# Performance work log

Measured on AMD Instinct MI355X. Metric: run time of the kernel, lower is better.

## Reference

```python
import jax, jax.numpy as jnp
import numpy as np

D2 = 200  # 2*D with D=100, hidden size of H and U

def setup_inputs() -> dict:
    key = jax.random.key(0)
    k1, k2, k3, k4 = jax.random.split(key, 4)
    B, T, J = 64, 2048, 128
    H = jax.random.normal(k1, (B, T, D2), dtype=jnp.float32)
    U = jax.random.normal(k2, (B, J, D2), dtype=jnp.float32)
    # alpha = nn.Linear(6D, 1): weight [600], bias scalar
    bound = 1.0 / np.sqrt(6 * 100)
    w = jax.random.uniform(k3, (3 * D2,), minval=-bound, maxval=bound, dtype=jnp.float32)
    b = jax.random.uniform(k4, (), minval=-bound, maxval=bound, dtype=jnp.float32)
    return {"H": H, "U": U, "w": w, "b": b}

def reference(H, U, w, b):
    # Trilinear similarity S[b,t,j] = alpha([H_t; U_j; H_t*U_j]) decomposed:
    # identical math to concat+linear, without materializing [B,T*J,6D].
    w_h, w_u, w_m = w[:D2], w[D2:2 * D2], w[2 * D2:]
    S = (jnp.einsum('btd,d->bt', H, w_h)[:, :, None]
         + jnp.einsum('bjd,d->bj', U, w_u)[:, None, :]
         + jnp.einsum('btd,d,bjd->btj', H, w_m, U)
         + b)  # [B,T,J]
    C2Q_att = jax.nn.softmax(S, axis=-1)            # [B,T,J]
    U_tilde = jnp.einsum('btj,bjd->btd', C2Q_att, U)  # [B,T,2D]
    Q2C_att = jax.nn.softmax(jnp.max(S, axis=-1), axis=-1)  # [B,T]
    H_tilde = jnp.einsum('bt,btd->bd', Q2C_att, H)[:, None, :]  # [B,1,2D]
    T = H.shape[1]
    H_tilde_rep = jnp.broadcast_to(H_tilde, H.shape)  # repeat(1,T,1)
    G = jnp.concatenate([H, U_tilde, H * U_tilde, H * H_tilde_rep], axis=-1)  # [B,T,8D]
    return G, Q2C_att[:, None, :]
```

## Files before the change

kernel.cpp:

```cpp
#include <hip/hip_runtime.h>
#include <math.h>

typedef __attribute__((ext_vector_type(8))) short bf16x8;
typedef __attribute__((ext_vector_type(4))) float f32x4;

#define Bb 64
#define Tt 2048
#define Jj 128
#define Dd 200
#define GD 800
#define TILE 32
#define NT 16
#define ROWS_BLK (TILE*NT)
#define NTH 1024

#define OFF_USH 0u
#define OFF_UJT 57344u
#define OFF_HMS 110592u
#define OFF_PSH 139264u
#define OFF_SUS 147456u
#define OFF_SHS 147968u
#define OFF_SMX 148224u
#define OFF_SSM 149248u
#define SMEM_BYTES 150272u

__device__ __forceinline__ unsigned short f2bf(float f) {
    union { float f; unsigned u; } v; v.f = f;
    unsigned r = v.u + 0x7FFFu + ((v.u >> 16) & 1u);
    return (unsigned short)(r >> 16);
}

__device__ __forceinline__ bf16x8 pack8(f32x4 a, f32x4 b) {
    bf16x8 o;
    o[0] = (short)f2bf(a[0]); o[1] = (short)f2bf(a[1]);
    o[2] = (short)f2bf(a[2]); o[3] = (short)f2bf(a[3]);
    o[4] = (short)f2bf(b[0]); o[5] = (short)f2bf(b[1]);
    o[6] = (short)f2bf(b[2]); o[7] = (short)f2bf(b[3]);
    return o;
}

__device__ __forceinline__ void stage_h(char* smem, const float* __restrict__ Hrows,
                                        int tid, int buf,
                                        f32x4 wmA, f32x4 wmB, f32x4 whA, f32x4 whB)
{
    const int row = tid >> 5, c = tid & 31;
    float shp = 0.f;
    bf16x8 val = {0,0,0,0,0,0,0,0};
    if (c < 25) {
        const float* p = Hrows + row * Dd + c * 8;
        f32x4 h0 = *(const f32x4*)p, h1 = *(const f32x4*)(p + 4);
        shp = h0[0]*whA[0] + h0[1]*whA[1] + h0[2]*whA[2] + h0[3]*whA[3]
            + h1[0]*whB[0] + h1[1]*whB[1] + h1[2]*whB[2] + h1[3]*whB[3];
        val = pack8(h0 * wmA, h1 * wmB);
    }
    if (c < 28) {
        unsigned a = OFF_HMS + (unsigned)buf * 14336u + (unsigned)row * 448u + (unsigned)c * 16u;
        *(bf16x8*)(smem + (a ^ ((unsigned)(row & 7) << 4))) = val;
    }
    #pragma unroll
    for (int off = 16; off; off >>= 1) shp += __shfl_xor(shp, off);
    if ((tid & 31) == 0)
        *(float*)(smem + OFF_SHS + (unsigned)buf * 128u + (unsigned)row * 4u) = shp;
}

__global__ __launch_bounds__(NTH) void k_main(
    const float* __restrict__ H, const float* __restrict__ U,
    const float* __restrict__ wt, const float* __restrict__ bptr,
    float* __restrict__ G, float* __restrict__ mrow)
{
    __shared__ __align__(16) char smem[SMEM_BYTES];

    const int tid  = threadIdx.x;
    const int lane = tid & 63;
    const int wv   = tid >> 6;

    const int swz = ((blockIdx.x & 7) << 5) | (blockIdx.x >> 3);
    const int b   = swz >> 2;
    const int t0  = (swz & 3) * ROWS_BLK;

    const float* Hb = H + ((size_t)b * Tt + t0) * Dd;
    const float* Ub = U + (size_t)b * Jj * Dd;
    const float  bb = bptr[0];

    const int cc = tid & 31;
    f32x4 whA = {0,0,0,0}, whB = {0,0,0,0}, wmA = {0,0,0,0}, wmB = {0,0,0,0};
    if (cc < 25) {
        whA = *(const f32x4*)(wt + cc * 8);       whB = *(const f32x4*)(wt + cc * 8 + 4);
        wmA = *(const f32x4*)(wt + 400 + cc * 8); wmB = *(const f32x4*)(wt + 400 + cc * 8 + 4);
    }
    const float wu0 = wt[200 + lane], wu1 = wt[264 + lane], wu2 = wt[328 + lane];
    const float wu3 = (lane < 8) ? wt[392 + lane] : 0.f;

    for (int i = tid; i < 128 * 28; i += NTH) {
        int row = i / 28, c8 = i % 28;
        bf16x8 val = {0,0,0,0,0,0,0,0};
        if (c8 < 25) {
            const float* p = Ub + row * Dd + c8 * 8;
            val = pack8(*(const f32x4*)p, *(const f32x4*)(p + 4));
        }
        unsigned a = OFF_USH + (unsigned)row * 448u + (unsigned)c8 * 16u;
        *(bf16x8*)(smem + (a ^ ((unsigned)(row & 7) << 4))) = val;
    }
    stage_h(smem, Hb, tid, 0, wmA, wmB, whA, whB);
    for (int jj = 0; jj < 8; ++jj) {
        int j = wv * 8 + jj;
        const float* up = Ub + j * Dd;
        float v = up[lane] * wu0 + up[64 + lane] * wu1 + up[128 + lane] * wu2;
        if (lane < 8) v += up[192 + lane] * wu3;
        #pragma unroll
        for (int off = 32; off; off >>= 1) v += __shfl_xor(v, off);
        if (lane == 0) *(float*)(smem + OFF_SUS + (unsigned)j * 4u) = v + bb;
    }
    __syncthreads();

    for (int i = tid; i < 208 * 64; i += NTH) {
        int d  = i >> 6;
        int jp = (i & 63) << 1;
        unsigned short v0 = 0, v1 = 0;
        if (d < Dd) {
            unsigned a0 = OFF_USH + (unsigned)jp * 448u + ((unsigned)d << 1);
            v0 = *(const unsigned short*)(smem + (a0 ^ ((unsigned)(jp & 7) << 4)));
            unsigned a1 = OFF_USH + (unsigned)(jp + 1) * 448u + ((unsigned)d << 1);
            v1 = *(const unsigned short*)(smem + (a1 ^ ((unsigned)((jp + 1) & 7) << 4)));
        }
        unsigned pk = (unsigned)v0 | ((unsigned)v1 << 16);
        unsigned wa = OFF_UJT + (unsigned)d * 256u + (unsigned)((i & 63) << 2);
        *(unsigned*)(smem + (wa ^ ((unsigned)(d & 7) << 4))) = pk;
    }

    const int rg  = wv >> 3;
    const int cg  = wv & 7;
    const int l15 = lane & 15;
    const int lq  = lane >> 4;
    const unsigned kfo = (unsigned)(lq << 4);
    const int rowA    = rg * 16 + l15;
    const int rowBase = rg * 16 + (lq << 2);
    const int jcol    = cg * 16 + l15;
    const int  dt0  = cg, dt1 = cg + 8;
    const bool has2 = (dt1 < 13);
    const int  dcol0 = dt0 * 16 + l15;
    const int  dcol1 = dt1 * 16 + l15;

    const unsigned hswz = (unsigned)(rowA & 7) << 4;
    const unsigned ubase = OFF_USH + (unsigned)jcol * 448u;
    const unsigned uswz  = (unsigned)(jcol & 7) << 4;
    const unsigned pbase = OFF_PSH + (unsigned)rowA * 256u;
    const unsigned pswz  = (unsigned)(rowA & 7) << 4;

    for (int tile = 0; tile < NT; ++tile) {
        const int cur = tile & 1, nxt = cur ^ 1;
        const float* Ht = Hb + (size_t)tile * TILE * Dd;

        if (tile + 1 < NT)
            stage_h(smem, Ht + TILE * Dd, tid, nxt, wmA, wmB, whA, whB);

        f32x4 acc = {0.f, 0.f, 0.f, 0.f};
        const unsigned hbase = OFF_HMS + (unsigned)cur * 14336u + (unsigned)rowA * 448u;
        #pragma unroll
        for (int ki = 0; ki < 7; ++ki) {
            bf16x8 af = *(const bf16x8*)(smem + ((hbase + (unsigned)ki * 64u + kfo) ^ hswz));
            bf16x8 bf = *(const bf16x8*)(smem + ((ubase + (unsigned)ki * 64u + kfo) ^ uswz));
            acc = __builtin_amdgcn_mfma_f32_16x16x32_bf16(af, bf, acc, 0, 0, 0);
        }

        const float suv = *(const float*)(smem + OFF_SUS + (unsigned)jcol * 4u);
        f32x4 sh4 = *(const f32x4*)(smem + OFF_SHS + (unsigned)cur * 128u + (unsigned)rowBase * 4u);
        float sv[4], ev[4], Mv[4];
        #pragma unroll
        for (int r = 0; r < 4; ++r) {
            float s = acc[r] + sh4[r] + suv;
            sv[r] = s;
            float m = s;
            m = fmaxf(m, __shfl_xor(m, 1));
            m = fmaxf(m, __shfl_xor(m, 2));
            m = fmaxf(m, __shfl_xor(m, 4));
            m = fmaxf(m, __shfl_xor(m, 8));
            if (l15 == 0)
                *(float*)(smem + OFF_SMX + (unsigned)((rowBase + r) * 8 + cg) * 4u) = m;
        }
        __syncthreads();
        #pragma unroll
        for (int r = 0; r < 4; ++r) {
            f32x4 ma = *(const f32x4*)(smem + OFF_SMX + (unsigned)(rowBase + r) * 32u);
            f32x4 mb2 = *(const f32x4*)(smem + OFF_SMX + (unsigned)(rowBase + r) * 32u + 16u);
            float M = fmaxf(fmaxf(fmaxf(ma[0], ma[1]), fmaxf(ma[2], ma[3])),
                            fmaxf(fmaxf(mb2[0], mb2[1]), fmaxf(mb2[2], mb2[3])));
            Mv[r] = M;
            float e = __expf(sv[r] - M);
            ev[r] = e;
            float ssum = e;
            ssum += __shfl_xor(ssum, 1); ssum += __shfl_xor(ssum, 2);
            ssum += __shfl_xor(ssum, 4); ssum += __shfl_xor(ssum, 8);
            if (l15 == 0)
                *(float*)(smem + OFF_SSM + (unsigned)((rowBase + r) * 8 + cg) * 4u) = ssum;
        }
        if (cg == 0 && l15 == 0) {
            #pragma unroll
            for (int r = 0; r < 4; ++r)
                mrow[(size_t)b * Tt + t0 + tile * TILE + rowBase + r] = Mv[r];
        }
        __syncthreads();
        #pragma unroll
        for (int r = 0; r < 4; ++r) {
            f32x4 sa = *(const f32x4*)(smem + OFF_SSM + (unsigned)(rowBase + r) * 32u);
            f32x4 sb = *(const f32x4*)(smem + OFF_SSM + (unsigned)(rowBase + r) * 32u + 16u);
            float inv = 1.f / (sa[0] + sa[1] + sa[2] + sa[3] + sb[0] + sb[1] + sb[2] + sb[3]);
            float p  = ev[r] * inv;
            float pn = __shfl_down(p, 1);
            if (!(lane & 1)) {
                int row = rowBase + r;
                unsigned a0 = OFF_PSH + (unsigned)row * 256u + (unsigned)jcol * 2u;
                *(unsigned*)(smem + (a0 ^ ((unsigned)(row & 7) << 4))) =
                    (unsigned)f2bf(p) | ((unsigned)f2bf(pn) << 16);
            }
        }
        __syncthreads();

        f32x4 acc0 = {0.f,0.f,0.f,0.f}, acc1 = {0.f,0.f,0.f,0.f};
        #pragma unroll
        for (int ki = 0; ki < 4; ++ki) {
            bf16x8 af = *(const bf16x8*)(smem + ((pbase + (unsigned)ki * 64u + kfo) ^ pswz));
            bf16x8 b0 = *(const bf16x8*)(smem +
                ((OFF_UJT + (unsigned)dcol0 * 256u + (unsigned)ki * 64u + kfo) ^ ((unsigned)(dcol0 & 7) << 4)));
            acc0 = __builtin_amdgcn_mfma_f32_16x16x32_bf16(af, b0, acc0, 0, 0, 0);
            if (has2) {
                bf16x8 b1 = *(const bf16x8*)(smem +
                    ((OFF_UJT + (unsigned)dcol1 * 256u + (unsigned)ki * 64u + kfo) ^ ((unsigned)(dcol1 & 7) << 4)));
                acc1 = __builtin_amdgcn_mfma_f32_16x16x32_bf16(af, b1, acc1, 0, 0, 0);
            }
        }

        float* Gtile = G + ((size_t)b * Tt + t0 + tile * TILE) * GD;
        #pragma unroll
        for (int r = 0; r < 4; ++r) {
            int row = rowBase + r;
            float* grow = Gtile + (size_t)row * GD;
            {
                float ut = acc0[r];
                float h  = Ht[row * Dd + dcol0];
                grow[200 + dcol0] = ut;
                grow[400 + dcol0] = h * ut;
            }
            if (has2 && dcol1 < Dd) {
                float ut = acc1[r];
                float h  = Ht[row * Dd + dcol1];
                grow[200 + dcol1] = ut;
                grow[400 + dcol1] = h * ut;
            }
        }
        for (int i = tid; i < TILE * 50; i += NTH) {
            int row = i / 50, c = i % 50;
            f32x4 h4 = *(const f32x4*)(Ht + row * Dd + c * 4);
            *(f32x4*)(Gtile + (size_t)row * GD + c * 4) = h4;
        }
    }
}

__global__ __launch_bounds__(256) void k_q(
    const float* __restrict__ mrow, float* __restrict__ q)
{
    __shared__ float red[4];
    __shared__ float sM, sS;
    const int b = blockIdx.x, tid = threadIdx.x;
    const int lane = tid & 63, wv = tid >> 6;
    const float* mb = mrow + (size_t)b * Tt;

    float lm = -1e30f;
    for (int i = tid; i < Tt; i += 256) lm = fmaxf(lm, mb[i]);
    #pragma unroll
    for (int off = 32; off; off >>= 1) lm = fmaxf(lm, __shfl_xor(lm, off));
    if (lane == 0) red[wv] = lm;
    __syncthreads();
    if (tid == 0) sM = fmaxf(fmaxf(red[0], red[1]), fmaxf(red[2], red[3]));
    __syncthreads();
    const float M = sM;

    float ls = 0.f;
    for (int i = tid; i < Tt; i += 256) ls += __expf(mb[i] - M);
    #pragma unroll
    for (int off = 32; off; off >>= 1) ls += __shfl_xor(ls, off);
    __syncthreads();
    if (lane == 0) red[wv] = ls;
    __syncthreads();
    if (tid == 0) sS = red[0] + red[1] + red[2] + red[3];
    __syncthreads();
    const float invS = 1.f / sS;

    for (int i = tid; i < Tt; i += 256)
        q[(size_t)b * Tt + i] = __expf(mb[i] - M) * invS;
}

__global__ __launch_bounds__(256) void k_ht(
    const float* __restrict__ H, const float* __restrict__ q,
    float* __restrict__ htil)
{
    const int b = blockIdx.y, ch = blockIdx.x;
    const int d4 = threadIdx.x & 63;
    const int tp = threadIdx.x >> 6;
    if (d4 >= 50) return;
    const float* Hb = H + (size_t)b * Tt * Dd;
    const float* qb = q + (size_t)b * Tt;
    f32x4 acc = {0.f, 0.f, 0.f, 0.f};
    const int tbase = ch * 128 + tp * 32;
    for (int k = 0; k < 32; ++k) {
        int t = tbase + k;
        f32x4 h4 = *(const f32x4*)(Hb + (size_t)t * Dd + d4 * 4);
        acc += h4 * qb[t];
    }
    float* hp = htil + b * Dd + d4 * 4;
    atomicAdd(hp + 0, acc[0]); atomicAdd(hp + 1, acc[1]);
    atomicAdd(hp + 2, acc[2]); atomicAdd(hp + 3, acc[3]);
}

__global__ __launch_bounds__(256) void k_g3(
    const float* __restrict__ H, const float* __restrict__ htil,
    float* __restrict__ G)
{
    const int idx = blockIdx.x * 256 + threadIdx.x;
    if (idx >= Bb * Tt * 50) return;
    const int d4 = idx % 50;
    const int bt = idx / 50;
    const int b  = bt >> 11;
    f32x4 h4 = *(const f32x4*)(H + (size_t)bt * Dd + d4 * 4);
    f32x4 t4 = *(const f32x4*)(htil + b * Dd + d4 * 4);
    *(f32x4*)(G + (size_t)bt * GD + 600 + d4 * 4) = h4 * t4;
}

extern "C" void kernel_launch(void* const* d_in, const int* in_sizes, int n_in,
                              void* d_out, int out_size, void* d_ws, size_t ws_size,
                              hipStream_t stream)
{
    const float* H    = (const float*)d_in[0];
    const float* U    = (const float*)d_in[1];
    const float* wt   = (const float*)d_in[2];
    const float* bptr = (const float*)d_in[3];

    float* G    = (float*)d_out;
    float* q    = G + (size_t)Bb * Tt * GD;
    float* mrow = (float*)d_ws;
    float* htil = mrow + (size_t)Bb * Tt;

    hipMemsetAsync(htil, 0, (size_t)Bb * Dd * sizeof(float), stream);

    k_main<<<(Bb * Tt / ROWS_BLK), NTH, 0, stream>>>(H, U, wt, bptr, G, mrow);

    k_q<<<Bb, 256, 0, stream>>>(mrow, q);

    dim3 g2(Tt / 128, Bb);
    k_ht<<<g2, 256, 0, stream>>>(H, q, htil);

    const int n3 = Bb * Tt * 50;
    k_g3<<<(n3 + 255) / 256, 256, 0, stream>>>(H, htil, G);
}
```

Baseline: 642.5 us.

## Prefetch next H tile into registers, reuse for G copy, fuse softmax into H-tilde kernel

The main kernel now splits H staging into a global load issued at the start of each tile and a shared-memory write at the end, so the next tile's load overlaps the MFMA and softmax work. The same registers are reused to write the H slice of G, which removes a second global read of H. The per-element H values needed for H*U_tilde are also loaded early. __syncthreads is replaced with an LDS-only wait plus barrier. Separately, the q softmax kernel is merged into the H-tilde reduction, each block recomputing the max and sum itself, which removes one launch but duplicates the reduction across 16 blocks per batch.

Result: faster. 596.3 us (-7.2%).

```diff
diff --git a/kernel.cpp b/kernel.cpp
--- a/kernel.cpp
+++ b/kernel.cpp
@@ -39,16 +39,31 @@
     return o;
 }
 
-__device__ __forceinline__ void stage_h(char* smem, const float* __restrict__ Hrows,
-                                        int tid, int buf,
-                                        f32x4 wmA, f32x4 wmB, f32x4 whA, f32x4 whB)
+__device__ __forceinline__ void bar_lds() {
+    asm volatile("s_waitcnt lgkmcnt(0)" ::: "memory");
+    __builtin_amdgcn_s_barrier();
+    asm volatile("" ::: "memory");
+}
+
+__device__ __forceinline__ void stage_load(const float* __restrict__ Hrows, int tid,
+                                           f32x4& h0, f32x4& h1)
+{
+    const int row = tid >> 5, c = tid & 31;
+    if (c < 25) {
+        const float* p = Hrows + row * Dd + c * 8;
+        h0 = *(const f32x4*)p;
+        h1 = *(const f32x4*)(p + 4);
+    }
+}
+
+__device__ __forceinline__ void stage_write(char* smem, int tid, int buf,
+                                            f32x4 h0, f32x4 h1,
+                                            f32x4 wmA, f32x4 wmB, f32x4 whA, f32x4 whB)
 {
     const int row = tid >> 5, c = tid & 31;
     float shp = 0.f;
     bf16x8 val = {0,0,0,0,0,0,0,0};
     if (c < 25) {
-        const float* p = Hrows + row * Dd + c * 8;
-        f32x4 h0 = *(const f32x4*)p, h1 = *(const f32x4*)(p + 4);
         shp = h0[0]*whA[0] + h0[1]*whA[1] + h0[2]*whA[2] + h0[3]*whA[3]
             + h1[0]*whB[0] + h1[1]*whB[1] + h1[2]*whB[2] + h1[3]*whB[3];
         val = pack8(h0 * wmA, h1 * wmB);
@@ -101,7 +116,9 @@
         unsigned a = OFF_USH + (unsigned)row * 448u + (unsigned)c8 * 16u;
         *(bf16x8*)(smem + (a ^ ((unsigned)(row & 7) << 4))) = val;
     }
-    stage_h(smem, Hb, tid, 0, wmA, wmB, whA, whB);
+    f32x4 pv0 = {0,0,0,0}, pv1 = {0,0,0,0};
+    stage_load(Hb, tid, pv0, pv1);
+    stage_write(smem, tid, 0, pv0, pv1, wmA, wmB, whA, whB);
     for (int jj = 0; jj < 8; ++jj) {
         int j = wv * 8 + jj;
         const float* up = Ub + j * Dd;
@@ -136,10 +153,11 @@
     const int rowA    = rg * 16 + l15;
     const int rowBase = rg * 16 + (lq << 2);
     const int jcol    = cg * 16 + l15;
-    const int  dt0  = cg, dt1 = cg + 8;
+    const int  dt1  = cg + 8;
     const bool has2 = (dt1 < 13);
-    const int  dcol0 = dt0 * 16 + l15;
+    const int  dcol0 = cg * 16 + l15;
     const int  dcol1 = dt1 * 16 + l15;
+    const bool use1  = has2 && (dcol1 < Dd);
 
     const unsigned hswz = (unsigned)(rowA & 7) << 4;
     const unsigned ubase = OFF_USH + (unsigned)jcol * 448u;
@@ -150,9 +168,16 @@
     for (int tile = 0; tile < NT; ++tile) {
         const int cur = tile & 1, nxt = cur ^ 1;
         const float* Ht = Hb + (size_t)tile * TILE * Dd;
-
-        if (tile + 1 < NT)
-            stage_h(smem, Ht + TILE * Dd, tid, nxt, wmA, wmB, whA, whB);
+        const bool havenext = (tile + 1 < NT);
+
+        f32x4 nh0 = {0,0,0,0}, nh1 = {0,0,0,0};
+        if (havenext) stage_load(Ht + TILE * Dd, tid, nh0, nh1);
+        float eh0[4], eh1[4];
+        #pragma unroll
+        for (int r = 0; r < 4; ++r) {
+            eh0[r] = Ht[(rowBase + r) * Dd + dcol0];
+            eh1[r] = use1 ? Ht[(rowBase + r) * Dd + dcol1] : 0.f;
+        }
 
         f32x4 acc = {0.f, 0.f, 0.f, 0.f};
         const unsigned hbase = OFF_HMS + (unsigned)cur * 14336u + (unsigned)rowA * 448u;
@@ -178,10 +203,10 @@
             if (l15 == 0)
                 *(float*)(smem + OFF_SMX + (unsigned)((rowBase + r) * 8 + cg) * 4u) = m;
         }
-        __syncthreads();
-        #pragma unroll
-        for (int r = 0; r < 4; ++r) {
-            f32x4 ma = *(const f32x4*)(smem + OFF_SMX + (unsigned)(rowBase + r) * 32u);
+        bar_lds();
+        #pragma unroll
+        for (int r = 0; r < 4; ++r) {
+            f32x4 ma  = *(const f32x4*)(smem + OFF_SMX + (unsigned)(rowBase + r) * 32u);
             f32x4 mb2 = *(const f32x4*)(smem + OFF_SMX + (unsigned)(rowBase + r) * 32u + 16u);
             float M = fmaxf(fmaxf(fmaxf(ma[0], ma[1]), fmaxf(ma[2], ma[3])),
                             fmaxf(fmaxf(mb2[0], mb2[1]), fmaxf(mb2[2], mb2[3])));
@@ -199,7 +224,7 @@
             for (int r = 0; r < 4; ++r)
                 mrow[(size_t)b * Tt + t0 + tile * TILE + rowBase + r] = Mv[r];
         }
-        __syncthreads();
+        bar_lds();
         #pragma unroll
         for (int r = 0; r < 4; ++r) {
             f32x4 sa = *(const f32x4*)(smem + OFF_SSM + (unsigned)(rowBase + r) * 32u);
@@ -214,7 +239,7 @@
                     (unsigned)f2bf(p) | ((unsigned)f2bf(pn) << 16);
             }
         }
-        __syncthreads();
+        bar_lds();
 
         f32x4 acc0 = {0.f,0.f,0.f,0.f}, acc1 = {0.f,0.f,0.f,0.f};
         #pragma unroll
@@ -230,46 +255,49 @@
             }
         }
 
-        float* Gtile = G + ((size_t)b * Tt + t0 + tile * TILE) * GD;
-        #pragma unroll
-        for (int r = 0; r < 4; ++r) {
-            int row = rowBase + r;
-            float* grow = Gtile + (size_t)row * GD;
-            {
-                float ut = acc0[r];
-                float h  = Ht[row * Dd + dcol0];
-                grow[200 + dcol0] = ut;
-                grow[400 + dcol0] = h * ut;
+        float* Gtile = G + ((size_t)b * Tt + t0 + (size_t)tile * TILE) * GD;
+        #pragma unroll
+        for (int r = 0; r < 4; ++r) {
+            float* grow = Gtile + (size_t)(rowBase + r) * GD;
+            grow[200 + dcol0] = acc0[r];
+            grow[400 + dcol0] = eh0[r] * acc0[r];
+            if (use1) {
+                grow[200 + dcol1] = acc1[r];
+                grow[400 + dcol1] = eh1[r] * acc1[r];
             }
-            if (has2 && dcol1 < Dd) {
-                float ut = acc1[r];
-                float h  = Ht[row * Dd + dcol1];
-                grow[200 + dcol1] = ut;
-                grow[400 + dcol1] = h * ut;
+        }
+        {
+            const int row = tid >> 5;
+            if (cc < 25) {
+                float* gp = Gtile + (size_t)row * GD + cc * 8;
+                *(f32x4*)gp       = pv0;
+                *(f32x4*)(gp + 4) = pv1;
             }
         }
-        for (int i = tid; i < TILE * 50; i += NTH) {
-            int row = i / 50, c = i % 50;
-            f32x4 h4 = *(const f32x4*)(Ht + row * Dd + c * 4);
-            *(f32x4*)(Gtile + (size_t)row * GD + c * 4) = h4;
-        }
-    }
-}
-
-__global__ __launch_bounds__(256) void k_q(
-    const float* __restrict__ mrow, float* __restrict__ q)
+
+        if (havenext) {
+            stage_write(smem, tid, nxt, nh0, nh1, wmA, wmB, whA, whB);
+            pv0 = nh0; pv1 = nh1;
+            bar_lds();
+        }
+    }
+}
+
+__global__ __launch_bounds__(256) void k_htq(
+    const float* __restrict__ H, const float* __restrict__ mrow,
+    float* __restrict__ q, float* __restrict__ htil)
 {
     __shared__ float red[4];
     __shared__ float sM, sS;
-    const int b = blockIdx.x, tid = threadIdx.x;
-    const int lane = tid & 63, wv = tid >> 6;
+    const int b = blockIdx.y, ch = blockIdx.x;
+    const int tid = threadIdx.x, lane = tid & 63, wvv = tid >> 6;
     const float* mb = mrow + (size_t)b * Tt;
 
     float lm = -1e30f;
     for (int i = tid; i < Tt; i += 256) lm = fmaxf(lm, mb[i]);
     #pragma unroll
     for (int off = 32; off; off >>= 1) lm = fmaxf(lm, __shfl_xor(lm, off));
-    if (lane == 0) red[wv] = lm;
+    if (lane == 0) red[wvv] = lm;
     __syncthreads();
     if (tid == 0) sM = fmaxf(fmaxf(red[0], red[1]), fmaxf(red[2], red[3]));
     __syncthreads();
@@ -280,33 +308,30 @@
     #pragma unroll
     for (int off = 32; off; off >>= 1) ls += __shfl_xor(ls, off);
     __syncthreads();
-    if (lane == 0) red[wv] = ls;
+    if (lane == 0) red[wvv] = ls;
     __syncthreads();
     if (tid == 0) sS = red[0] + red[1] + red[2] + red[3];
     __syncthreads();
     const float invS = 1.f / sS;
 
-    for (int i = tid; i < Tt; i += 256)
-        q[(size_t)b * Tt + i] = __expf(mb[i] - M) * invS;
-}
-
-__global__ __launch_bounds__(256) void k_ht(
-    const float* __restrict__ H, const float* __restrict__ q,
-    float* __restrict__ htil)
-{
-    const int b = blockIdx.y, ch = blockIdx.x;
-    const int d4 = threadIdx.x & 63;
-    const int tp = threadIdx.x >> 6;
+    if (ch == 0) {
+        for (int i = tid; i < Tt; i += 256)
+            q[(size_t)b * Tt + i] = __expf(mb[i] - M) * invS;
+    }
+
+    const int d4 = tid & 63;
+    const int tp = tid >> 6;
     if (d4 >= 50) return;
     const float* Hb = H + (size_t)b * Tt * Dd;
-    const float* qb = q + (size_t)b * Tt;
     f32x4 acc = {0.f, 0.f, 0.f, 0.f};
     const int tbase = ch * 128 + tp * 32;
     for (int k = 0; k < 32; ++k) {
         int t = tbase + k;
+        float p = __expf(mb[t] - M);
         f32x4 h4 = *(const f32x4*)(Hb + (size_t)t * Dd + d4 * 4);
-        acc += h4 * qb[t];
-    }
+        acc += h4 * p;
+    }
+    acc *= invS;
     float* hp = htil + b * Dd + d4 * 4;
     atomicAdd(hp + 0, acc[0]); atomicAdd(hp + 1, acc[1]);
     atomicAdd(hp + 2, acc[2]); atomicAdd(hp + 3, acc[3]);
@@ -344,10 +369,8 @@
 
     k_main<<<(Bb * Tt / ROWS_BLK), NTH, 0, stream>>>(H, U, wt, bptr, G, mrow);
 
-    k_q<<<Bb, 256, 0, stream>>>(mrow, q);
-
     dim3 g2(Tt / 128, Bb);
-    k_ht<<<g2, 256, 0, stream>>>(H, q, htil);
+    k_htq<<<g2, 256, 0, stream>>>(H, mrow, q, htil);
 
     const int n3 = Bb * Tt * 50;
     k_g3<<<(n3 + 255) / 256, 256, 0, stream>>>(H, htil, G);
```
